# Kernel optimization log

Measured on AMD Instinct MI355X. Metric: run time of the kernel, lower is better.

Reference implementation:

```python
import jax, jax.numpy as jnp
import numpy as np

N = 50000      # num_nodes
E = 800000     # num_edges
D_IN = 128
D_HID = 128
D_EMB = 128
G = 4          # num_gcns
BN_EPS = 1e-5


def setup_inputs() -> dict:
    key = jax.random.key(0)
    ks = jax.random.split(key, 8)
    x = jax.random.normal(ks[0], (N, D_IN), dtype=jnp.float32)
    edge_index = jax.random.randint(ks[1], (2, E), 0, N, dtype=jnp.int64)
    # per-GCN params, stacked on leading G axis
    W1 = jax.random.normal(ks[2], (G, D_IN, D_HID), dtype=jnp.float32) / np.sqrt(D_IN)
    b1 = jnp.zeros((G, D_HID), dtype=jnp.float32)
    W2 = jax.random.normal(ks[3], (G, D_HID, D_EMB), dtype=jnp.float32) / np.sqrt(D_HID)
    b2 = jnp.zeros((G, D_EMB), dtype=jnp.float32)
    gamma1 = jnp.ones((G, D_HID), dtype=jnp.float32)
    beta1 = jnp.zeros((G, D_HID), dtype=jnp.float32)
    gamma2 = jnp.ones((G, D_EMB), dtype=jnp.float32)
    beta2 = jnp.zeros((G, D_EMB), dtype=jnp.float32)
    alpha = jnp.asarray(0.25, dtype=jnp.float32)  # PReLU (single shared param)
    mix_embed = jnp.full((N, G), 1.0 / G, dtype=jnp.float32)
    return {"x": x, "edge_index": edge_index, "W1": W1, "b1": b1, "W2": W2,
            "b2": b2, "gamma1": gamma1, "beta1": beta1, "gamma2": gamma2,
            "beta2": beta2, "alpha": alpha, "mix_embed": mix_embed}


def _gcn_norm(edge_index, num_nodes):
    # PyG GCNConv: add self-loops, symmetric normalization D^-1/2 (A+I) D^-1/2
    row, col = edge_index[0], edge_index[1]
    loop = jnp.arange(num_nodes, dtype=edge_index.dtype)
    row = jnp.concatenate([row, loop])
    col = jnp.concatenate([col, loop])
    w = jnp.ones(row.shape[0], dtype=jnp.float32)
    deg = jax.ops.segment_sum(w, col, num_segments=num_nodes)
    dinv = jnp.where(deg > 0, deg ** -0.5, 0.0)
    norm = dinv[row] * w * dinv[col]
    return row, col, norm


def _propagate(h, row, col, norm, num_nodes):
    # gather from source, scale by edge norm, scatter-add to target
    msg = h[row] * norm[:, None]
    return jax.ops.segment_sum(msg, col, num_segments=num_nodes)


def _batchnorm(z, gamma, beta):
    mu = jnp.mean(z, axis=0)
    var = jnp.mean((z - mu) ** 2, axis=0)  # biased, as torch BN training mode
    return (z - mu) * jax.lax.rsqrt(var + BN_EPS) * gamma + beta


def _prelu(z, alpha):
    return jnp.where(z > 0, z, alpha * z)


def reference(x, edge_index, W1, b1, W2, b2, gamma1, beta1, gamma2, beta2, alpha, mix_embed):
    num_nodes = x.shape[0]
    row, col, norm = _gcn_norm(edge_index, num_nodes)
    mix = jax.nn.softmax(mix_embed, axis=-1)  # [N, G]
    out = jnp.zeros((num_nodes, D_EMB), dtype=x.dtype)
    for g in range(G):  # small fixed number of mixture components
        h = x @ W1[g]
        z = _propagate(h, row, col, norm, num_nodes) + b1[g]
        z = _prelu(_batchnorm(z, gamma1[g], beta1[g]), alpha)
        h = z @ W2[g]
        z = _propagate(h, row, col, norm, num_nodes) + b2[g]
        z = _prelu(_batchnorm(z, gamma2[g], beta2[g]), alpha)
        out = out + mix[:, g:g + 1] * z
    return out
```

## Files before the change

### kernel.cpp

```cpp
#include <hip/hip_runtime.h>
#include <stdint.h>

static constexpr float EPS = 1e-5f;

typedef __attribute__((ext_vector_type(8))) short bfrag;
typedef __attribute__((ext_vector_type(4))) float ffrag;

__device__ __forceinline__ float bf2f(unsigned short u){
  union { unsigned int i; float f; } v; v.i = ((unsigned int)u) << 16; return v.f;
}
__device__ __forceinline__ unsigned short f2bf(float f){
  union { float f; unsigned int i; } v; v.f = f;
  unsigned int x = v.i;
  x += 0x7fffu + ((x >> 16) & 1u);
  return (unsigned short)(x >> 16);
}
__device__ __forceinline__ float lo16(unsigned int v){ return bf2f((unsigned short)(v & 0xffffu)); }
__device__ __forceinline__ float hi16(unsigned int v){ return bf2f((unsigned short)(v >> 16)); }
__device__ __forceinline__ unsigned int pack2(float a, float b){
  return ((unsigned int)f2bf(b) << 16) | (unsigned int)f2bf(a);
}

__global__ __launch_bounds__(256) void k_deg(const int* __restrict__ col, int* __restrict__ indeg,
                                             int N, int E, int dbl,
                                             const float* __restrict__ W1, const float* __restrict__ W2,
                                             unsigned short* __restrict__ Wt1, unsigned short* __restrict__ Wt2){
  int b = blockIdx.x;
  if (b < dbl){
    int e0 = (b * 256 + threadIdx.x) * 2;
    if (e0 < E){
      if (e0 + 1 < E){
        int2 cc = *(const int2*)&col[e0];
        unsigned c0 = (unsigned)cc.x, c1 = (unsigned)cc.y;
        if (c0 < (unsigned)N) atomicAdd(&indeg[c0], 1);
        if (c1 < (unsigned)N) atomicAdd(&indeg[c1], 1);
      } else {
        unsigned c0 = (unsigned)col[e0];
        if (c0 < (unsigned)N) atomicAdd(&indeg[c0], 1);
      }
    }
  } else {
    int idx = (b - dbl) * 256 + threadIdx.x;
    const float* W = W1; unsigned short* Wt = Wt1;
    if (idx >= 65536){ idx -= 65536; W = W2; Wt = Wt2; }
    int c = idx >> 7, k = idx & 127;
    int g = c >> 7, j = c & 127;
    Wt[(size_t)c * 128 + k] = f2bf(W[(size_t)g*16384 + k*128 + j]);
  }
}

__global__ void k_alloc(const int* __restrict__ indeg, int* __restrict__ ctr,
                        int* __restrict__ offs, int* __restrict__ cursor,
                        float* __restrict__ dinv, int N){
  int tid = blockIdx.x * 256 + threadIdx.x;
  int lane = threadIdx.x & 63;
  int v = (tid < N) ? indeg[tid] : 0;
  int incl = v;
  #pragma unroll
  for (int d = 1; d < 64; d <<= 1){
    int u = __shfl_up(incl, d);
    if (lane >= d) incl += u;
  }
  int base = 0;
  if (lane == 63) base = atomicAdd(ctr, incl);
  base = __shfl(base, 63);
  if (tid < N){
    int o = base + incl - v;
    offs[tid] = o; cursor[tid] = o;
    dinv[tid] = rsqrtf((float)(v + 1));
  }
}

__global__ __launch_bounds__(256) void k_scatter(const int* __restrict__ row, const int* __restrict__ col,
                                                 int* __restrict__ cursor, int* __restrict__ csr,
                                                 int N, int E, int sbl,
                                                 const float* __restrict__ x, const float* __restrict__ dinv,
                                                 unsigned short* __restrict__ xs, int total4x){
  int b = blockIdx.x;
  if (b < sbl){
    int e0 = (b * 256 + threadIdx.x) * 2;
    #pragma unroll
    for (int q = 0; q < 2; q++){
      int e = e0 + q;
      if (e < E){
        unsigned c = (unsigned)col[e];
        if (c < (unsigned)N){
          int p = atomicAdd(&cursor[c], 1);
          unsigned r = (unsigned)row[e];
          csr[p] = (r < (unsigned)N) ? (int)r : 0;
        }
      }
    }
  } else {
    int idx = (b - sbl) * 256 + threadIdx.x;
    int stride = (gridDim.x - sbl) * 256;
    for (; idx < total4x; idx += stride){
      int i = idx >> 5;
      float di = dinv[i];
      float4 v = ((const float4*)x)[idx];
      ushort4 o;
      o.x = f2bf(di * v.x); o.y = f2bf(di * v.y);
      o.z = f2bf(di * v.z); o.w = f2bf(di * v.w);
      ((ushort4*)xs)[idx] = o;
    }
  }
}

__global__ __launch_bounds__(256) void k_prop_x(const unsigned int* __restrict__ xs2,
                                               const int* __restrict__ csr,
                                               const int* __restrict__ offs, const int* __restrict__ indeg,
                                               const float* __restrict__ dinv,
                                               unsigned int* __restrict__ s2, int N){
  int i = blockIdx.x * 4 + (threadIdx.x >> 6);
  if (i >= N) return;
  int c2 = threadIdx.x & 63;
  unsigned int sv = xs2[(size_t)i*64 + c2];
  float ax = lo16(sv), ay = hi16(sv);
  int e = offs[i], end = e + indeg[i];
  for (; e + 8 <= end; e += 8){
    int r0 = csr[e], r1 = csr[e+1], r2 = csr[e+2], r3 = csr[e+3];
    int r4 = csr[e+4], r5 = csr[e+5], r6 = csr[e+6], r7 = csr[e+7];
    unsigned int v0 = xs2[(size_t)r0*64 + c2], v1 = xs2[(size_t)r1*64 + c2];
    unsigned int v2 = xs2[(size_t)r2*64 + c2], v3 = xs2[(size_t)r3*64 + c2];
    unsigned int v4 = xs2[(size_t)r4*64 + c2], v5 = xs2[(size_t)r5*64 + c2];
    unsigned int v6 = xs2[(size_t)r6*64 + c2], v7 = xs2[(size_t)r7*64 + c2];
    ax += lo16(v0)+lo16(v1)+lo16(v2)+lo16(v3)+lo16(v4)+lo16(v5)+lo16(v6)+lo16(v7);
    ay += hi16(v0)+hi16(v1)+hi16(v2)+hi16(v3)+hi16(v4)+hi16(v5)+hi16(v6)+hi16(v7);
  }
  for (; e < end; e++){
    unsigned int v = xs2[(size_t)csr[e]*64 + c2];
    ax += lo16(v); ay += hi16(v);
  }
  float di = dinv[i];
  s2[(size_t)i*64 + c2] = pack2(di * ax, di * ay);
}

__global__ __launch_bounds__(256) void k_gram(const unsigned short* __restrict__ in,
                                              int rstride, int coff128,
                                              float* __restrict__ Gbase, float* __restrict__ msumbase,
                                              int N){
  int gy = blockIdx.y;
  const unsigned short* src = in + gy * coff128;
  float* G = Gbase + (size_t)gy * 16384;
  float* msum = msumbase + gy * 128;

  __shared__ unsigned short st[128 * 40];
  __shared__ float colsum[128];

  int t = threadIdx.x;
  int wv = t >> 6, lane = t & 63, l16 = lane & 15, quad = lane >> 4;
  if (t < 128) colsum[t] = 0.f;

  int sn = t & 31, scb = t >> 5;

  ffrag acc[2][8];
  #pragma unroll
  for (int a = 0; a < 2; a++)
    #pragma unroll
    for (int b = 0; b < 8; b++) acc[a][b] = (ffrag){0.f,0.f,0.f,0.f};

  float cs[16];
  #pragma unroll
  for (int j = 0; j < 16; j++) cs[j] = 0.f;

  for (int c0 = blockIdx.x * 32; c0 < N; c0 += gridDim.x * 32){
    __syncthreads();
    int n = c0 + sn;
    ushort4 u0, u1, u2, u3;
    if (n < N){
      const ushort4* p = (const ushort4*)(src + (size_t)n * rstride + scb * 16);
      u0 = p[0]; u1 = p[1]; u2 = p[2]; u3 = p[3];
    } else {
      u0 = u1 = u2 = u3 = (ushort4){0,0,0,0};
    }
    unsigned short vals[16] = {u0.x,u0.y,u0.z,u0.w, u1.x,u1.y,u1.z,u1.w,
                               u2.x,u2.y,u2.z,u2.w, u3.x,u3.y,u3.z,u3.w};
    #pragma unroll
    for (int j = 0; j < 16; j++){
      st[(scb * 16 + j) * 40 + sn] = vals[j];
      cs[j] += bf2f(vals[j]);
    }
    __syncthreads();
    #pragma unroll
    for (int ta = 0; ta < 2; ta++){
      int ra = wv * 2 + ta;
      bfrag af = *(const bfrag*)&st[(ra * 16 + l16) * 40 + quad * 8];
      #pragma unroll
      for (int tb = 0; tb < 8; tb++){
        bfrag bf = *(const bfrag*)&st[(tb * 16 + l16) * 40 + quad * 8];
        acc[ta][tb] = __builtin_amdgcn_mfma_f32_16x16x32_bf16(af, bf, acc[ta][tb], 0, 0, 0);
      }
    }
  }
  #pragma unroll
  for (int j = 0; j < 16; j++) atomicAdd(&colsum[scb * 16 + j], cs[j]);
  __syncthreads();
  if (t < 128) atomicAdd(&msum[t], colsum[t]);
  #pragma unroll
  for (int ta = 0; ta < 2; ta++){
    #pragma unroll
    for (int tb = 0; tb < 8; tb++){
      int row0 = wv * 32 + ta * 16 + quad * 4;
      int colg = tb * 16 + l16;
      #pragma unroll
      for (int r = 0; r < 4; r++)
        atomicAdd(&G[(size_t)(row0 + r) * 128 + colg], acc[ta][tb][r]);
    }
  }
}

__global__ __launch_bounds__(64) void k_bnfit(const float* __restrict__ W,
                                              const float* __restrict__ gamma, const float* __restrict__ beta,
                                              const float* __restrict__ Gbase, int gmul,
                                              const float* __restrict__ msumbase, int mmul,
                                              float* __restrict__ scale, float* __restrict__ shiftF,
                                              float invN){
  int c = blockIdx.x;
  int g = c >> 7, j = c & 127;
  const float* Wc = W + (size_t)g * 16384 + j;
  const float* G  = Gbase + (size_t)g * gmul;
  const float* mv = msumbase + g * mmul;
  __shared__ float wl[128];
  __shared__ float ml[128];
  int t = threadIdx.x;
  for (int k = t; k < 128; k += 64){ wl[k] = Wc[(size_t)k * 128]; ml[k] = mv[k] * invN; }
  __syncthreads();
  float quad = 0.f, dm = 0.f;
  #pragma unroll
  for (int kk = 0; kk < 2; kk++){
    int k = t + kk * 64;
    float wk = wl[k];
    dm += ml[k] * wk;
    const float* Gr = G + (size_t)k * 128;
    float p = 0.f;
    for (int jj = 0; jj < 128; jj += 4){
      float4 gg = *(const float4*)(Gr + jj);
      float4 ww = *(const float4*)(wl + jj);
      p += gg.x*ww.x + gg.y*ww.y + gg.z*ww.z + gg.w*ww.w;
    }
    quad += wk * p;
  }
  for (int o = 32; o > 0; o >>= 1){
    quad += __shfl_down(quad, o);
    dm   += __shfl_down(dm, o);
  }
  if (t == 0){
    float var = quad * invN - dm * dm;
    float sc = gamma[c] * rsqrtf(var + EPS);
    scale[c] = sc;
    shiftF[c] = beta[c] - dm * sc;
  }
}

__global__ __launch_bounds__(256) void k_mm1f(const unsigned short* __restrict__ in,
                                              const unsigned short* __restrict__ Wt,
                                              const float* __restrict__ scale, const float* __restrict__ shiftF,
                                              const float* __restrict__ alpha_p, const float* __restrict__ dinv,
                                              unsigned short* __restrict__ h, int N){
  float alpha = alpha_p[0];
  int wave = threadIdx.x >> 6, lane = threadIdx.x & 63;
  int l16 = lane & 15, quad = lane >> 4;
  int node = blockIdx.x * 16 + l16;
  int nc = node < N ? node : N - 1;
  int colbase0 = wave * 128;
  float di = dinv[nc];

  const unsigned short* inrow = in + (size_t)nc * 128 + quad * 8;
  bfrag b0 = *(const bfrag*)(inrow);
  bfrag b1 = *(const bfrag*)(inrow + 32);
  bfrag b2 = *(const bfrag*)(inrow + 64);
  bfrag b3 = *(const bfrag*)(inrow + 96);

  #pragma unroll
  for (int ct = 0; ct < 8; ct++){
    int colbase = colbase0 + ct * 16;
    const unsigned short* wrow = Wt + (size_t)(colbase + l16) * 128 + quad * 8;
    bfrag a0 = *(const bfrag*)(wrow);
    bfrag a1 = *(const bfrag*)(wrow + 32);
    bfrag a2 = *(const bfrag*)(wrow + 64);
    bfrag a3 = *(const bfrag*)(wrow + 96);
    ffrag acc = {0.f, 0.f, 0.f, 0.f};
    acc = __builtin_amdgcn_mfma_f32_16x16x32_bf16(a0, b0, acc, 0, 0, 0);
    acc = __builtin_amdgcn_mfma_f32_16x16x32_bf16(a1, b1, acc, 0, 0, 0);
    acc = __builtin_amdgcn_mfma_f32_16x16x32_bf16(a2, b2, acc, 0, 0, 0);
    acc = __builtin_amdgcn_mfma_f32_16x16x32_bf16(a3, b3, acc, 0, 0, 0);
    int cb = colbase + quad * 4;
    float4 sc = *(const float4*)(scale + cb);
    float4 sh = *(const float4*)(shiftF + cb);
    float v0 = acc[0]*sc.x + sh.x; v0 = v0 > 0.f ? v0 : alpha*v0;
    float v1 = acc[1]*sc.y + sh.y; v1 = v1 > 0.f ? v1 : alpha*v1;
    float v2 = acc[2]*sc.z + sh.z; v2 = v2 > 0.f ? v2 : alpha*v2;
    float v3 = acc[3]*sc.w + sh.w; v3 = v3 > 0.f ? v3 : alpha*v3;
    uint2 o;
    o.x = pack2(di*v0, di*v1);
    o.y = pack2(di*v2, di*v3);
    if (node < N)
      *(uint2*)(h + (size_t)node * 512 + cb) = o;
  }
}

__global__ __launch_bounds__(256) void k_prop_h(const unsigned int* __restrict__ h2,
                                                const int* __restrict__ csr,
                                                const int* __restrict__ offs, const int* __restrict__ indeg,
                                                const float* __restrict__ dinv,
                                                unsigned int* __restrict__ t2, int N){
  int i = blockIdx.x;
  int c2 = threadIdx.x;
  unsigned int sv = h2[(size_t)i*256 + c2];
  float ax = lo16(sv), ay = hi16(sv);
  int e = offs[i], end = e + indeg[i];
  for (; e + 16 <= end; e += 16){
    int r[16];
    #pragma unroll
    for (int j = 0; j < 16; j++) r[j] = csr[e + j];
    unsigned int v[16];
    #pragma unroll
    for (int j = 0; j < 16; j++) v[j] = h2[(size_t)r[j]*256 + c2];
    #pragma unroll
    for (int j = 0; j < 16; j++){ ax += lo16(v[j]); ay += hi16(v[j]); }
  }
  for (; e + 4 <= end; e += 4){
    int r0 = csr[e], r1 = csr[e+1], r2 = csr[e+2], r3 = csr[e+3];
    unsigned int v0 = h2[(size_t)r0*256 + c2], v1 = h2[(size_t)r1*256 + c2];
    unsigned int v2 = h2[(size_t)r2*256 + c2], v3 = h2[(size_t)r3*256 + c2];
    ax += lo16(v0)+lo16(v1)+lo16(v2)+lo16(v3);
    ay += hi16(v0)+hi16(v1)+hi16(v2)+hi16(v3);
  }
  for (; e < end; e++){
    unsigned int v = h2[(size_t)csr[e]*256 + c2];
    ax += lo16(v); ay += hi16(v);
  }
  float di = dinv[i];
  t2[(size_t)i*256 + c2] = pack2(di * ax, di * ay);
}

__global__ __launch_bounds__(256) void k_mm2f(const unsigned short* __restrict__ t,
                                              const unsigned short* __restrict__ Wt,
                                              const float* __restrict__ scale, const float* __restrict__ shiftF,
                                              const float* __restrict__ alpha_p, const float* __restrict__ mixe,
                                              float* __restrict__ out, int N){
  __shared__ float red[4][16][132];
  float alpha = alpha_p[0];
  int wave = threadIdx.x >> 6, lane = threadIdx.x & 63;
  int l16 = lane & 15, quad = lane >> 4;
  int node = blockIdx.x * 16 + l16;
  int nc = node < N ? node : N - 1;

  float4 me = ((const float4*)mixe)[nc];
  float mx = fmaxf(fmaxf(me.x, me.y), fmaxf(me.z, me.w));
  float e0 = __expf(me.x - mx), e1 = __expf(me.y - mx), e2 = __expf(me.z - mx), e3 = __expf(me.w - mx);
  float inv = 1.f / (e0 + e1 + e2 + e3);
  float wvx = ((wave == 0) ? e0 : (wave == 1) ? e1 : (wave == 2) ? e2 : e3) * inv;

  const unsigned short* inrow = t + (size_t)nc * 512 + wave * 128 + quad * 8;
  bfrag b0 = *(const bfrag*)(inrow);
  bfrag b1 = *(const bfrag*)(inrow + 32);
  bfrag b2 = *(const bfrag*)(inrow + 64);
  bfrag b3 = *(const bfrag*)(inrow + 96);

  #pragma unroll
  for (int ct = 0; ct < 8; ct++){
    int c512 = wave * 128 + ct * 16;
    const unsigned short* wrow = Wt + (size_t)(c512 + l16) * 128 + quad * 8;
    bfrag a0 = *(const bfrag*)(wrow);
    bfrag a1 = *(const bfrag*)(wrow + 32);
    bfrag a2 = *(const bfrag*)(wrow + 64);
    bfrag a3 = *(const bfrag*)(wrow + 96);
    ffrag acc = {0.f, 0.f, 0.f, 0.f};
    acc = __builtin_amdgcn_mfma_f32_16x16x32_bf16(a0, b0, acc, 0, 0, 0);
    acc = __builtin_amdgcn_mfma_f32_16x16x32_bf16(a1, b1, acc, 0, 0, 0);
    acc = __builtin_amdgcn_mfma_f32_16x16x32_bf16(a2, b2, acc, 0, 0, 0);
    acc = __builtin_amdgcn_mfma_f32_16x16x32_bf16(a3, b3, acc, 0, 0, 0);
    int cb = c512 + quad * 4;
    float4 sc = *(const float4*)(scale + cb);
    float4 sh = *(const float4*)(shiftF + cb);
    float v0 = acc[0]*sc.x + sh.x; v0 = v0 > 0.f ? v0 : alpha*v0;
    float v1 = acc[1]*sc.y + sh.y; v1 = v1 > 0.f ? v1 : alpha*v1;
    float v2 = acc[2]*sc.z + sh.z; v2 = v2 > 0.f ? v2 : alpha*v2;
    float v3 = acc[3]*sc.w + sh.w; v3 = v3 > 0.f ? v3 : alpha*v3;
    int j = ct * 16 + quad * 4;
    float4 wr = {wvx*v0, wvx*v1, wvx*v2, wvx*v3};
    *(float4*)&red[wave][l16][j] = wr;
  }
  __syncthreads();
  int tt = threadIdx.x;
  int nn = tt >> 4, j0 = (tt & 15) * 8;
  int gnode = blockIdx.x * 16 + nn;
  if (gnode < N){
    float4 r0 = {0,0,0,0}, r1 = {0,0,0,0};
    #pragma unroll
    for (int w = 0; w < 4; w++){
      float4 p0 = *(const float4*)&red[w][nn][j0];
      float4 p1 = *(const float4*)&red[w][nn][j0 + 4];
      r0.x += p0.x; r0.y += p0.y; r0.z += p0.z; r0.w += p0.w;
      r1.x += p1.x; r1.y += p1.y; r1.z += p1.z; r1.w += p1.w;
    }
    float* op = out + (size_t)gnode * 128 + j0;
    *(float4*)(op) = r0;
    *(float4*)(op + 4) = r1;
  }
}

extern "C" void kernel_launch(void* const* d_in, const int* in_sizes, int n_in,
                              void* d_out, int out_size, void* d_ws, size_t ws_size,
                              hipStream_t stream) {
  const float* x      = (const float*)d_in[0];
  const int*   ei     = (const int*)d_in[1];
  const float* W1     = (const float*)d_in[2];
  const float* W2     = (const float*)d_in[4];
  const float* gamma1 = (const float*)d_in[6];
  const float* beta1  = (const float*)d_in[7];
  const float* gamma2 = (const float*)d_in[8];
  const float* beta2  = (const float*)d_in[9];
  const float* alpha  = (const float*)d_in[10];
  const float* mixe   = (const float*)d_in[11];
  float* out = (float*)d_out;

  const int N = in_sizes[0] / 128;
  const int E = in_sizes[1] / 2;
  const int* rowv = ei;
  const int* colv = ei + E;

  char* w = (char*)d_ws;
  size_t off = 0;
  auto take = [&](size_t bytes) -> void* {
    void* p = w + off;
    off = (off + bytes + 255) & ~(size_t)255;
    return p;
  };
  size_t zbeg = off;
  int*   indeg  = (int*)take((size_t)N * 4);
  int*   ctr    = (int*)take(256);
  float* G1     = (float*)take(65536);
  float* G2     = (float*)take(262144);
  float* m1     = (float*)take(512);
  float* m2     = (float*)take(2048);
  size_t zend = off;
  int*   cursor = (int*)take((size_t)N * 4);
  int*   offs   = (int*)take((size_t)N * 4);
  float* dinv   = (float*)take((size_t)N * 4);
  float* scale1 = (float*)take(2048);
  float* shift1 = (float*)take(2048);
  float* scale2 = (float*)take(2048);
  float* shift2 = (float*)take(2048);
  int*   csr    = (int*)take((size_t)E * 4);
  unsigned short* Wt1 = (unsigned short*)take(512 * 128 * 2);
  unsigned short* Wt2 = (unsigned short*)take(512 * 128 * 2);
  unsigned short* xs = (unsigned short*)take((size_t)N * 128 * 2);
  unsigned short* sb = (unsigned short*)take((size_t)N * 128 * 2);
  unsigned short* h  = (unsigned short*)take((size_t)N * 512 * 2);
  unsigned short* tb = (unsigned short*)take((size_t)N * 512 * 2);

  hipMemsetAsync((char*)d_ws + zbeg, 0, zend - zbeg, stream);

  int nb  = (N + 255) / 256;
  int dbl = (E + 511) / 512;
  float invN = 1.0f / (float)N;

  k_deg<<<dbl + 512, 256, 0, stream>>>(colv, indeg, N, E, dbl, W1, W2, Wt1, Wt2);
  k_alloc<<<nb, 256, 0, stream>>>(indeg, ctr, offs, cursor, dinv, N);
  k_scatter<<<dbl + 1024, 256, 0, stream>>>(rowv, colv, cursor, csr, N, E, dbl, x, dinv, xs, N * 32);

  k_prop_x<<<(N + 3) / 4, 256, 0, stream>>>((const unsigned int*)xs, csr, offs, indeg, dinv, (unsigned int*)sb, N);

  k_gram<<<dim3(32, 1), 256, 0, stream>>>(sb, 128, 0, G1, m1, N);
  k_bnfit<<<512, 64, 0, stream>>>(W1, gamma1, beta1, G1, 0, m1, 0, scale1, shift1, invN);
  k_mm1f<<<(N + 15) / 16, 256, 0, stream>>>(sb, Wt1, scale1, shift1, alpha, dinv, h, N);

  k_prop_h<<<N, 256, 0, stream>>>((const unsigned int*)h, csr, offs, indeg, dinv, (unsigned int*)tb, N);

  k_gram<<<dim3(32, 4), 256, 0, stream>>>(tb, 512, 128, G2, m2, N);
  k_bnfit<<<512, 64, 0, stream>>>(W2, gamma2, beta2, G2, 16384, m2, 128, scale2, shift2, invN);
  k_mm2f<<<(N + 15) / 16, 256, 0, stream>>>(tb, Wt2, scale2, shift2, alpha, mixe, out, N);
}
```

Baseline: 604.5 us.

## Replace Gram atomics with per-block partials and reduce; remap prop_h to 4 nodes per block

The Gram kernel now runs twice as many blocks. Each block writes its 128x128 partial Gram matrix to its own slot instead of doing global atomicAdds, and a new k_gred kernel sums the partials. This removes atomic contention on G and doubles the parallelism of the Gram pass, at the cost of extra partial-buffer traffic and one more launch. Separately, k_prop_h now has each 256-thread block cover four nodes with a 64-column slice each, instead of one node with all 256 columns, which changes wave-level gather locality and the block count.

```diff
diff --git a/kernel.cpp b/kernel.cpp
--- a/kernel.cpp
+++ b/kernel.cpp
@@ -2,6 +2,7 @@
 #include <stdint.h>
 
 static constexpr float EPS = 1e-5f;
+static constexpr int XB = 64;
 
 typedef __attribute__((ext_vector_type(8))) short bfrag;
 typedef __attribute__((ext_vector_type(4))) float ffrag;
@@ -137,11 +138,11 @@
 
 __global__ __launch_bounds__(256) void k_gram(const unsigned short* __restrict__ in,
                                               int rstride, int coff128,
-                                              float* __restrict__ Gbase, float* __restrict__ msumbase,
+                                              float* __restrict__ Gpart, float* __restrict__ msumbase,
                                               int N){
   int gy = blockIdx.y;
   const unsigned short* src = in + gy * coff128;
-  float* G = Gbase + (size_t)gy * 16384;
+  float* Gp = Gpart + ((size_t)gy * XB + blockIdx.x) * 16384;
   float* msum = msumbase + gy * 128;
 
   __shared__ unsigned short st[128 * 40];
@@ -204,9 +205,19 @@
       int colg = tb * 16 + l16;
       #pragma unroll
       for (int r = 0; r < 4; r++)
-        atomicAdd(&G[(size_t)(row0 + r) * 128 + colg], acc[ta][tb][r]);
-    }
-  }
+        Gp[(size_t)(row0 + r) * 128 + colg] = acc[ta][tb][r];
+    }
+  }
+}
+
+__global__ __launch_bounds__(256) void k_gred(const float* __restrict__ Gpart, float* __restrict__ G){
+  int i = blockIdx.x * 256 + threadIdx.x;
+  int grp = blockIdx.y;
+  const float* src = Gpart + (size_t)grp * XB * 16384;
+  float s = 0.f;
+  #pragma unroll 4
+  for (int xb = 0; xb < XB; xb++) s += src[(size_t)xb * 16384 + i];
+  G[(size_t)grp * 16384 + i] = s;
 }
 
 __global__ __launch_bounds__(64) void k_bnfit(const float* __restrict__ W,
@@ -304,8 +315,11 @@
                                                 const int* __restrict__ offs, const int* __restrict__ indeg,
                                                 const float* __restrict__ dinv,
                                                 unsigned int* __restrict__ t2, int N){
-  int i = blockIdx.x;
-  int c2 = threadIdx.x;
+  int B = blockIdx.x;
+  int s = B & 3;
+  int i = (B >> 2) * 4 + (threadIdx.x >> 6);
+  if (i >= N) return;
+  int c2 = s * 64 + (threadIdx.x & 63);
   unsigned int sv = h2[(size_t)i*256 + c2];
   float ax = lo16(sv), ay = hi16(sv);
   int e = offs[i], end = e + indeg[i];
@@ -431,11 +445,12 @@
   size_t zbeg = off;
   int*   indeg  = (int*)take((size_t)N * 4);
   int*   ctr    = (int*)take(256);
-  float* G1     = (float*)take(65536);
-  float* G2     = (float*)take(262144);
   float* m1     = (float*)take(512);
   float* m2     = (float*)take(2048);
   size_t zend = off;
+  float* G1     = (float*)take(65536);
+  float* G2     = (float*)take(262144);
+  float* Gpart  = (float*)take((size_t)4 * XB * 16384 * 4);
   int*   cursor = (int*)take((size_t)N * 4);
   int*   offs   = (int*)take((size_t)N * 4);
   float* dinv   = (float*)take((size_t)N * 4);
@@ -463,13 +478,15 @@
 
   k_prop_x<<<(N + 3) / 4, 256, 0, stream>>>((const unsigned int*)xs, csr, offs, indeg, dinv, (unsigned int*)sb, N);
 
-  k_gram<<<dim3(32, 1), 256, 0, stream>>>(sb, 128, 0, G1, m1, N);
+  k_gram<<<dim3(XB, 1), 256, 0, stream>>>(sb, 128, 0, Gpart, m1, N);
+  k_gred<<<dim3(64, 1), 256, 0, stream>>>(Gpart, G1);
   k_bnfit<<<512, 64, 0, stream>>>(W1, gamma1, beta1, G1, 0, m1, 0, scale1, shift1, invN);
   k_mm1f<<<(N + 15) / 16, 256, 0, stream>>>(sb, Wt1, scale1, shift1, alpha, dinv, h, N);
 
-  k_prop_h<<<N, 256, 0, stream>>>((const unsigned int*)h, csr, offs, indeg, dinv, (unsigned int*)tb, N);
-
-  k_gram<<<dim3(32, 4), 256, 0, stream>>>(tb, 512, 128, G2, m2, N);
+  k_prop_h<<<((N + 3) / 4) * 4, 256, 0, stream>>>((const unsigned int*)h, csr, offs, indeg, dinv, (unsigned int*)tb, N);
+
+  k_gram<<<dim3(XB, 4), 256, 0, stream>>>(tb, 512, 128, Gpart, m2, N);
+  k_gred<<<dim3(64, 4), 256, 0, stream>>>(Gpart, G2);
   k_bnfit<<<512, 64, 0, stream>>>(W2, gamma2, beta2, G2, 16384, m2, 128, scale2, shift2, invN);
   k_mm2f<<<(N + 15) / 16, 256, 0, stream>>>(tb, Wt2, scale2, shift2, alpha, mixe, out, N);
 }
```

Result: faster. 568.7 us (-5.9%).
